# Performance work log

Measured on AMD Instinct MI355X. Metric: run time of the kernel, lower is better.

The kernel has to match this reference:

```python
import jax, jax.numpy as jnp
import numpy as np
from jax import lax

B, T, D, H = 128, 1024, 512, 512

def setup_inputs() -> dict:
    key = jax.random.key(0)
    k1, k2, k3 = jax.random.split(key, 3)
    sx = 1.0 / np.sqrt(D)
    sh = 1.0 / np.sqrt(H)
    return {
        "x": jax.random.normal(k1, (B, T, D), dtype=jnp.float32),
        "Wx": jax.random.normal(k2, (D, 4 * H), dtype=jnp.float32) * sx,
        "Wh": jax.random.normal(k3, (H, 4 * H), dtype=jnp.float32) * sh,
        "b": jnp.zeros((4 * H,), dtype=jnp.float32),
    }

def reference(x, Wx, Wh, b):
    # x: (B, T, D). Standard LSTM recurrence over time via lax.scan.
    batch = x.shape[0]
    hid = Wh.shape[0]
    h0 = jnp.zeros((batch, hid), dtype=x.dtype)
    c0 = jnp.zeros((batch, hid), dtype=x.dtype)
    # Precompute input projections for all timesteps (one big GEMM).
    xg = jnp.einsum('btd,dg->btg', x, Wx) + b  # (B, T, 4H)
    xg_t = jnp.transpose(xg, (1, 0, 2))        # (T, B, 4H)

    def step(carry, xg_step):
        h, c = carry
        gates = xg_step + h @ Wh               # (B, 4H)
        i, f, g, o = jnp.split(gates, 4, axis=-1)
        i = jax.nn.sigmoid(i)
        f = jax.nn.sigmoid(f)
        g = jnp.tanh(g)
        o = jax.nn.sigmoid(o)
        c_new = f * c + i * g
        h_new = o * jnp.tanh(c_new)
        return (h_new, c_new), h_new

    (final_h, final_c), _ = lax.scan(step, (h0, c0), xg_t)
    # return_sequences=False -> final hidden state
    return final_h
```

## Files before the change

### kernel.cpp

```cpp
#include <hip/hip_runtime.h>


typedef _Float16 f16;
typedef _Float16 f16x2 __attribute__((ext_vector_type(2)));
typedef _Float16 f16x8 __attribute__((ext_vector_type(8)));
typedef float f32x4 __attribute__((ext_vector_type(4)));
typedef unsigned u32x4 __attribute__((ext_vector_type(4)));

#define MFMA16(a, b, c) __builtin_amdgcn_mfma_f32_16x16x32_f16(a, b, c, 0, 0, 0)

__device__ __forceinline__ float sigf(float x) { return 1.0f / (1.0f + __expf(-x)); }
__device__ __forceinline__ float tanh_fast(float x) { return 1.0f - 2.0f / (__expf(2.0f * x) + 1.0f); }

#define OFF_WXT   0ull
#define OFF_WHT   2097152ull
#define OFF_HBUF  4194304ull
#define OFF_CST   4718592ull
#define OFF_XG    5242880ull

__global__ __launch_bounds__(256) void prep_kernel(
    const float* __restrict__ Wx, const float* __restrict__ Wh,
    f16* __restrict__ wxT, f16* __restrict__ whT,
    f16* __restrict__ hbuf, float* __restrict__ cst)
{
    unsigned i = blockIdx.x * 256u + threadIdx.x;
    if (i < 1048576u) {
        unsigned g = i >> 9, d = i & 511u;
        wxT[i] = (f16)Wx[d * 2048u + g];
        whT[i] = (f16)Wh[d * 2048u + g];
    }
    if (i < 131072u)
        ((unsigned*)hbuf)[i] = (i < 32768u) ? 0u : 0xFFFFFFFFu;
    if (i < 65536u) cst[i] = 0.0f;
}

__global__ __launch_bounds__(256) void gemm_xg(
    const float* __restrict__ x, const f16* __restrict__ wxT,
    const float* __restrict__ bias, f16* __restrict__ xg,
    int t0, int tcLog)
{
    __shared__ f16 smem[16384];
    f16* As = smem;
    f16* Bs = smem + 4096;

    const int tid = threadIdx.x;
    const int lane = tid & 63, wid = tid >> 6;
    const int wm = wid >> 1, wn = wid & 1;
    const int lr = lane & 15, lh = lane >> 4;
    const int n0 = blockIdx.x * 128;
    const long m0 = (long)blockIdx.y * 128;

    const int srow = tid >> 1;
    const int sc0_ = (tid & 1) * 2;
    const int swz = (srow >> 1) & 3;

    const long mg = m0 + srow;
    const long bb = mg >> tcLog;
    const long tl = mg & ((1L << tcLog) - 1);
    const float* xrow = x + ((bb * 1024 + t0 + tl) * 512 + sc0_ * 8);
    const f16* brow = wxT + ((long)(n0 + srow) * 512 + sc0_ * 8);

    f32x4 acc[4][4] = {};

    for (int k0 = 0; k0 < 512; k0 += 32) {
        __syncthreads();
        float4 a0 = *(const float4*)(xrow + k0);
        float4 a1 = *(const float4*)(xrow + k0 + 4);
        float4 a2 = *(const float4*)(xrow + k0 + 8);
        float4 a3 = *(const float4*)(xrow + k0 + 12);
        f16x8 ha, hb;
        ha[0] = (f16)a0.x; ha[1] = (f16)a0.y; ha[2] = (f16)a0.z; ha[3] = (f16)a0.w;
        ha[4] = (f16)a1.x; ha[5] = (f16)a1.y; ha[6] = (f16)a1.z; ha[7] = (f16)a1.w;
        hb[0] = (f16)a2.x; hb[1] = (f16)a2.y; hb[2] = (f16)a2.z; hb[3] = (f16)a2.w;
        hb[4] = (f16)a3.x; hb[5] = (f16)a3.y; hb[6] = (f16)a3.z; hb[7] = (f16)a3.w;
        *(f16x8*)(As + srow * 32 + ((sc0_    ) ^ swz) * 8) = ha;
        *(f16x8*)(As + srow * 32 + ((sc0_ + 1) ^ swz) * 8) = hb;
        f16x8 b0 = *(const f16x8*)(brow + k0);
        f16x8 b1 = *(const f16x8*)(brow + k0 + 8);
        *(f16x8*)(Bs + srow * 32 + ((sc0_    ) ^ swz) * 8) = b0;
        *(f16x8*)(Bs + srow * 32 + ((sc0_ + 1) ^ swz) * 8) = b1;
        __syncthreads();

        f16x8 af[4], bf[4];
        #pragma unroll
        for (int fm = 0; fm < 4; fm++) {
            int r = wm * 64 + fm * 16 + lr;
            af[fm] = *(const f16x8*)(As + r * 32 + (lh ^ ((r >> 1) & 3)) * 8);
        }
        #pragma unroll
        for (int fn = 0; fn < 4; fn++) {
            int r = wn * 64 + fn * 16 + lr;
            bf[fn] = *(const f16x8*)(Bs + r * 32 + (lh ^ ((r >> 1) & 3)) * 8);
        }
        #pragma unroll
        for (int fm = 0; fm < 4; fm++)
            #pragma unroll
            for (int fn = 0; fn < 4; fn++)
                acc[fm][fn] = MFMA16(af[fm], bf[fn], acc[fm][fn]);
    }

    __syncthreads();
    f16* Os = smem;
    #pragma unroll
    for (int fn = 0; fn < 4; fn++) {
        float bv = bias[n0 + wn * 64 + fn * 16 + lr];
        #pragma unroll
        for (int fm = 0; fm < 4; fm++) {
            #pragma unroll
            for (int r = 0; r < 4; r++) {
                int row = wm * 64 + fm * 16 + lh * 4 + r;
                int col = wn * 64 + fn * 16 + lr;
                Os[row * 128 + col] = (f16)(acc[fm][fn][r] + bv);
            }
        }
    }
    __syncthreads();
    const int orow = tid >> 1;
    const int ocol = (tid & 1) * 64;
    f16* dst = xg + (m0 + orow) * 2048 + n0 + ocol;
    const f16* srcp = Os + orow * 128 + ocol;
    #pragma unroll
    for (int j = 0; j < 8; j++)
        *(uint4*)(dst + j * 8) = *(const uint4*)(srcp + j * 8);
}

__global__ __launch_bounds__(256, 1) void lstm_rec(
    const f16* __restrict__ whT, const f16* __restrict__ xg,
    f16* __restrict__ hbuf, float* __restrict__ cst,
    float* __restrict__ out, int t0, int tcLog)
{
    __shared__ unsigned short hA[16 * 520];
    __shared__ float gl[2048];
    const int tid = threadIdx.x;
    const int lane = tid & 63, w = tid >> 6;
    const int lr = lane & 15, lh = lane >> 4;
    const int g = blockIdx.x & 7, s = blockIdx.x >> 3;
    const int Tc = 1 << tcLog;

    f16x8 breg[2][16];
    #pragma unroll
    for (int fn = 0; fn < 2; fn++) {
        const f16* wp = whT + (long)(w * 512 + s * 32 + fn * 16 + lr) * 512 + lh * 8;
        #pragma unroll
        for (int ks = 0; ks < 16; ks++)
            breg[fn][ks] = *(const f16x8*)(wp + ks * 32);
    }

    const int pb = tid >> 4;
    const int pu = (tid & 15) * 2;
    const int bg = g * 16 + pb;
    const int hcol = s * 32 + pu;
    float2 cc = *(const float2*)(cst + bg * 512 + hcol);

    const int r_ = lane >> 2, cq_ = lane & 3;
    const long goff = (long)(g * 16 + r_) * 512 + w * 128 + cq_ * 8;

    const f16* xbase = xg + ((long)(bg << tcLog)) * 2048 + hcol;
    f16x2 xv0 = *(const f16x2*)(xbase);
    f16x2 xv1 = *(const f16x2*)(xbase + 512);
    f16x2 xv2 = *(const f16x2*)(xbase + 1024);
    f16x2 xv3 = *(const f16x2*)(xbase + 1536);

    for (int t = 0; t < Tc; t++) {
        const int tt = t0 + t;

        const f16* gq = hbuf + (tt & 3) * 65536 + goff;
        f16x8 q0, q1, q2, q3;
        int guard = 0;
        for (;;) {
            asm volatile("global_load_dwordx4 %0, %1, off sc0 sc1" : "=v"(q0) : "v"(gq) : "memory");
            asm volatile("global_load_dwordx4 %0, %1, off sc0 sc1" : "=v"(q1) : "v"(gq + 32) : "memory");
            asm volatile("global_load_dwordx4 %0, %1, off sc0 sc1" : "=v"(q2) : "v"(gq + 64) : "memory");
            asm volatile("global_load_dwordx4 %0, %1, off sc0 sc1" : "=v"(q3) : "v"(gq + 96) : "memory");
            asm volatile("s_waitcnt vmcnt(0)" ::: "memory");
            __builtin_amdgcn_sched_barrier(0);
            unsigned mx = 0u;
            {
                u32x4 u = __builtin_bit_cast(u32x4, q0);
                asm("v_pk_max_u16 %0, %0, %1" : "+v"(mx) : "v"(u.x));
                asm("v_pk_max_u16 %0, %0, %1" : "+v"(mx) : "v"(u.y));
                asm("v_pk_max_u16 %0, %0, %1" : "+v"(mx) : "v"(u.z));
                asm("v_pk_max_u16 %0, %0, %1" : "+v"(mx) : "v"(u.w));
            }
            {
                u32x4 u = __builtin_bit_cast(u32x4, q1);
                asm("v_pk_max_u16 %0, %0, %1" : "+v"(mx) : "v"(u.x));
                asm("v_pk_max_u16 %0, %0, %1" : "+v"(mx) : "v"(u.y));
                asm("v_pk_max_u16 %0, %0, %1" : "+v"(mx) : "v"(u.z));
                asm("v_pk_max_u16 %0, %0, %1" : "+v"(mx) : "v"(u.w));
            }
            {
                u32x4 u = __builtin_bit_cast(u32x4, q2);
                asm("v_pk_max_u16 %0, %0, %1" : "+v"(mx) : "v"(u.x));
                asm("v_pk_max_u16 %0, %0, %1" : "+v"(mx) : "v"(u.y));
                asm("v_pk_max_u16 %0, %0, %1" : "+v"(mx) : "v"(u.z));
                asm("v_pk_max_u16 %0, %0, %1" : "+v"(mx) : "v"(u.w));
            }
            {
                u32x4 u = __builtin_bit_cast(u32x4, q3);
                asm("v_pk_max_u16 %0, %0, %1" : "+v"(mx) : "v"(u.x));
                asm("v_pk_max_u16 %0, %0, %1" : "+v"(mx) : "v"(u.y));
                asm("v_pk_max_u16 %0, %0, %1" : "+v"(mx) : "v"(u.z));
                asm("v_pk_max_u16 %0, %0, %1" : "+v"(mx) : "v"(u.w));
            }
            int ok = ((mx & 0xFFFFu) != 0xFFFFu) && ((mx >> 16) != 0xFFFFu);
            if (__all(ok) || ++guard > 5000) break;
        }

        {
            unsigned short* dst = hA + r_ * 520 + w * 128 + cq_ * 8;
            *(f16x8*)(dst     ) = q0;
            *(f16x8*)(dst + 32) = q1;
            *(f16x8*)(dst + 64) = q2;
            *(f16x8*)(dst + 96) = q3;
        }
        __syncthreads();

        {
            f16* pz = hbuf + ((tt + 2) & 3) * 65536 + bg * 512 + hcol;
            unsigned cany = 0xFFFFFFFFu;
            asm volatile("global_store_dword %0, %1, off sc0 sc1"
                         :: "v"(pz), "v"(cany) : "memory");
        }

        f32x4 acc0 = {0.f, 0.f, 0.f, 0.f}, acc1 = {0.f, 0.f, 0.f, 0.f};
        #pragma unroll
        for (int ks = 0; ks < 16; ks++) {
            f16x8 a = *(const f16x8*)(hA + lr * 520 + lh * 8 + ks * 32);
            acc0 = MFMA16(a, breg[0][ks], acc0);
            acc1 = MFMA16(a, breg[1][ks], acc1);
        }
        #pragma unroll
        for (int r = 0; r < 4; r++) {
            gl[w * 512 + (lh * 4 + r) * 32 + lr] = acc0[r];
            gl[w * 512 + (lh * 4 + r) * 32 + 16 + lr] = acc1[r];
        }
        __syncthreads();

        float2 gi = *(const float2*)(gl + 0 * 512 + pb * 32 + pu);
        float2 gf = *(const float2*)(gl + 1 * 512 + pb * 32 + pu);
        float2 gg = *(const float2*)(gl + 2 * 512 + pb * 32 + pu);
        float2 go = *(const float2*)(gl + 3 * 512 + pb * 32 + pu);
        float i0 = sigf(gi.x + (float)xv0[0]);
        float i1 = sigf(gi.y + (float)xv0[1]);
        float f0 = sigf(gf.x + (float)xv1[0]);
        float f1 = sigf(gf.y + (float)xv1[1]);
        float g0 = tanh_fast(gg.x + (float)xv2[0]);
        float g1 = tanh_fast(gg.y + (float)xv2[1]);
        float o0 = sigf(go.x + (float)xv3[0]);
        float o1 = sigf(go.y + (float)xv3[1]);
        cc.x = f0 * cc.x + i0 * g0;
        cc.y = f1 * cc.y + i1 * g1;
        float h0 = o0 * tanh_fast(cc.x);
        float h1 = o1 * tanh_fast(cc.y);

        asm volatile("s_waitcnt vmcnt(0)" ::: "memory");
        {
            f16* hd = hbuf + ((tt + 1) & 3) * 65536 + bg * 512 + hcol;
            union { f16x2 h; unsigned u; } cv;
            cv.h[0] = (f16)h0; cv.h[1] = (f16)h1;
            asm volatile("global_store_dword %0, %1, off sc0 sc1"
                         :: "v"(hd), "v"(cv.u) : "memory");
        }
        if (tt == 1023) *(float2*)(out + bg * 512 + hcol) = make_float2(h0, h1);

        if (t + 1 < Tc) {
            const f16* xr = xbase + (long)(t + 1) * 2048;
            xv0 = *(const f16x2*)(xr);
            xv1 = *(const f16x2*)(xr + 512);
            xv2 = *(const f16x2*)(xr + 1024);
            xv3 = *(const f16x2*)(xr + 1536);
        }
    }
    *(float2*)(cst + bg * 512 + hcol) = cc;
}

extern "C" void kernel_launch(void* const* d_in, const int* in_sizes, int n_in,
                              void* d_out, int out_size, void* d_ws, size_t ws_size,
                              hipStream_t stream)
{
    const float* x    = (const float*)d_in[0];
    const float* Wx   = (const float*)d_in[1];
    const float* Wh   = (const float*)d_in[2];
    const float* bias = (const float*)d_in[3];
    float* out = (float*)d_out;
    char* ws = (char*)d_ws;

    f16*      wxT   = (f16*)(ws + OFF_WXT);
    f16*      whT   = (f16*)(ws + OFF_WHT);
    f16*      hbuf  = (f16*)(ws + OFF_HBUF);
    float*    cst   = (float*)(ws + OFF_CST);
    f16*      xgb   = (f16*)(ws + OFF_XG);

    int tcLog = 10;
    while (tcLog > 0 && OFF_XG + (524288ull << tcLog) > ws_size) tcLog--;
    const int nch = 1024 >> tcLog;

    prep_kernel<<<4096, 256, 0, stream>>>(Wx, Wh, wxT, whT, hbuf, cst);

    for (int c = 0; c < nch; c++) {
        int t0 = c << tcLog;
        dim3 gA(16, 1u << tcLog);
        gemm_xg<<<gA, 256, 0, stream>>>(x, wxT, bias, xgb, t0, tcLog);

        const f16* whT_a = whT; const f16* xg_a = xgb; f16* hbuf_a = hbuf;
        float* cst_a = cst; float* out_a = out;
        int t0_a = t0, tcl_a = tcLog;
        void* args[7] = { &whT_a, &xg_a, &hbuf_a, &cst_a, &out_a, &t0_a, &tcl_a };
        if (hipLaunchCooperativeKernel((const void*)lstm_rec, dim3(128), dim3(256),
                                       args, 0, stream) != hipSuccess) {
            lstm_rec<<<dim3(128), dim3(256), 0, stream>>>(whT, xgb, hbuf, cst, out, t0, tcLog);
        }
    }
}
```

Measured before the change: 3.424 ms.

## Deepen h ring buffer to 8 slots, drop store fence, pad gate LDS

Grows the global hidden-state ring buffer from 4 to 8 slots and invalidates the slot three steps ahead instead of two. This lets the s_waitcnt vmcnt(0) before the h store be removed, since the sentinel write and the data write can no longer race on the same slot. It also pads the gate scratch in LDS to a stride of 33 to avoid bank conflicts, at the cost of splitting each float2 read into scalar reads. The memory layout offsets move to make room for the larger buffer.

```diff
diff --git a/kernel.cpp b/kernel.cpp
--- a/kernel.cpp
+++ b/kernel.cpp
@@ -15,8 +15,8 @@
 #define OFF_WXT   0ull
 #define OFF_WHT   2097152ull
 #define OFF_HBUF  4194304ull
-#define OFF_CST   4718592ull
-#define OFF_XG    5242880ull
+#define OFF_CST   5242880ull
+#define OFF_XG    5505024ull
 
 __global__ __launch_bounds__(256) void prep_kernel(
     const float* __restrict__ Wx, const float* __restrict__ Wh,
@@ -29,7 +29,7 @@
         wxT[i] = (f16)Wx[d * 2048u + g];
         whT[i] = (f16)Wh[d * 2048u + g];
     }
-    if (i < 131072u)
+    if (i < 262144u)
         ((unsigned*)hbuf)[i] = (i < 32768u) ? 0u : 0xFFFFFFFFu;
     if (i < 65536u) cst[i] = 0.0f;
 }
@@ -124,13 +124,20 @@
         *(uint4*)(dst + j * 8) = *(const uint4*)(srcp + j * 8);
 }
 
+#define VALIDATE16(mx, q)                                            \
+    {  u32x4 u = __builtin_bit_cast(u32x4, q);                       \
+       asm("v_pk_max_u16 %0, %0, %1" : "+v"(mx) : "v"(u.x));         \
+       asm("v_pk_max_u16 %0, %0, %1" : "+v"(mx) : "v"(u.y));         \
+       asm("v_pk_max_u16 %0, %0, %1" : "+v"(mx) : "v"(u.z));         \
+       asm("v_pk_max_u16 %0, %0, %1" : "+v"(mx) : "v"(u.w));  }
+
 __global__ __launch_bounds__(256, 1) void lstm_rec(
     const f16* __restrict__ whT, const f16* __restrict__ xg,
     f16* __restrict__ hbuf, float* __restrict__ cst,
     float* __restrict__ out, int t0, int tcLog)
 {
     __shared__ unsigned short hA[16 * 520];
-    __shared__ float gl[2048];
+    __shared__ float gl[4 * 528];
     const int tid = threadIdx.x;
     const int lane = tid & 63, w = tid >> 6;
     const int lr = lane & 15, lh = lane >> 4;
@@ -164,7 +171,7 @@
     for (int t = 0; t < Tc; t++) {
         const int tt = t0 + t;
 
-        const f16* gq = hbuf + (tt & 3) * 65536 + goff;
+        const f16* gq = hbuf + (tt & 7) * 65536 + goff;
         f16x8 q0, q1, q2, q3;
         int guard = 0;
         for (;;) {
@@ -175,34 +182,7 @@
             asm volatile("s_waitcnt vmcnt(0)" ::: "memory");
             __builtin_amdgcn_sched_barrier(0);
             unsigned mx = 0u;
-            {
-                u32x4 u = __builtin_bit_cast(u32x4, q0);
-                asm("v_pk_max_u16 %0, %0, %1" : "+v"(mx) : "v"(u.x));
-                asm("v_pk_max_u16 %0, %0, %1" : "+v"(mx) : "v"(u.y));
-                asm("v_pk_max_u16 %0, %0, %1" : "+v"(mx) : "v"(u.z));
-                asm("v_pk_max_u16 %0, %0, %1" : "+v"(mx) : "v"(u.w));
-            }
-            {
-                u32x4 u = __builtin_bit_cast(u32x4, q1);
-                asm("v_pk_max_u16 %0, %0, %1" : "+v"(mx) : "v"(u.x));
-                asm("v_pk_max_u16 %0, %0, %1" : "+v"(mx) : "v"(u.y));
-                asm("v_pk_max_u16 %0, %0, %1" : "+v"(mx) : "v"(u.z));
-                asm("v_pk_max_u16 %0, %0, %1" : "+v"(mx) : "v"(u.w));
-            }
-            {
-                u32x4 u = __builtin_bit_cast(u32x4, q2);
-                asm("v_pk_max_u16 %0, %0, %1" : "+v"(mx) : "v"(u.x));
-                asm("v_pk_max_u16 %0, %0, %1" : "+v"(mx) : "v"(u.y));
-                asm("v_pk_max_u16 %0, %0, %1" : "+v"(mx) : "v"(u.z));
-                asm("v_pk_max_u16 %0, %0, %1" : "+v"(mx) : "v"(u.w));
-            }
-            {
-                u32x4 u = __builtin_bit_cast(u32x4, q3);
-                asm("v_pk_max_u16 %0, %0, %1" : "+v"(mx) : "v"(u.x));
-                asm("v_pk_max_u16 %0, %0, %1" : "+v"(mx) : "v"(u.y));
-                asm("v_pk_max_u16 %0, %0, %1" : "+v"(mx) : "v"(u.z));
-                asm("v_pk_max_u16 %0, %0, %1" : "+v"(mx) : "v"(u.w));
-            }
+            VALIDATE16(mx, q0) VALIDATE16(mx, q1) VALIDATE16(mx, q2) VALIDATE16(mx, q3)
             int ok = ((mx & 0xFFFFu) != 0xFFFFu) && ((mx >> 16) != 0xFFFFu);
             if (__all(ok) || ++guard > 5000) break;
         }
@@ -217,7 +197,7 @@
         __syncthreads();
 
         {
-            f16* pz = hbuf + ((tt + 2) & 3) * 65536 + bg * 512 + hcol;
+            f16* pz = hbuf + ((tt + 3) & 7) * 65536 + bg * 512 + hcol;
             unsigned cany = 0xFFFFFFFFu;
             asm volatile("global_store_dword %0, %1, off sc0 sc1"
                          :: "v"(pz), "v"(cany) : "memory");
@@ -232,31 +212,30 @@
         }
         #pragma unroll
         for (int r = 0; r < 4; r++) {
-            gl[w * 512 + (lh * 4 + r) * 32 + lr] = acc0[r];
-            gl[w * 512 + (lh * 4 + r) * 32 + 16 + lr] = acc1[r];
-        }
-        __syncthreads();
-
-        float2 gi = *(const float2*)(gl + 0 * 512 + pb * 32 + pu);
-        float2 gf = *(const float2*)(gl + 1 * 512 + pb * 32 + pu);
-        float2 gg = *(const float2*)(gl + 2 * 512 + pb * 32 + pu);
-        float2 go = *(const float2*)(gl + 3 * 512 + pb * 32 + pu);
-        float i0 = sigf(gi.x + (float)xv0[0]);
-        float i1 = sigf(gi.y + (float)xv0[1]);
-        float f0 = sigf(gf.x + (float)xv1[0]);
-        float f1 = sigf(gf.y + (float)xv1[1]);
-        float g0 = tanh_fast(gg.x + (float)xv2[0]);
-        float g1 = tanh_fast(gg.y + (float)xv2[1]);
-        float o0 = sigf(go.x + (float)xv3[0]);
-        float o1 = sigf(go.y + (float)xv3[1]);
+            gl[w * 528 + (lh * 4 + r) * 33 + lr] = acc0[r];
+            gl[w * 528 + (lh * 4 + r) * 33 + 16 + lr] = acc1[r];
+        }
+        __syncthreads();
+
+        float gi0 = gl[0 * 528 + pb * 33 + pu], gi1 = gl[0 * 528 + pb * 33 + pu + 1];
+        float gf0 = gl[1 * 528 + pb * 33 + pu], gf1 = gl[1 * 528 + pb * 33 + pu + 1];
+        float gg0 = gl[2 * 528 + pb * 33 + pu], gg1 = gl[2 * 528 + pb * 33 + pu + 1];
+        float go0 = gl[3 * 528 + pb * 33 + pu], go1 = gl[3 * 528 + pb * 33 + pu + 1];
+        float i0 = sigf(gi0 + (float)xv0[0]);
+        float i1 = sigf(gi1 + (float)xv0[1]);
+        float f0 = sigf(gf0 + (float)xv1[0]);
+        float f1 = sigf(gf1 + (float)xv1[1]);
+        float g0 = tanh_fast(gg0 + (float)xv2[0]);
+        float g1 = tanh_fast(gg1 + (float)xv2[1]);
+        float o0 = sigf(go0 + (float)xv3[0]);
+        float o1 = sigf(go1 + (float)xv3[1]);
         cc.x = f0 * cc.x + i0 * g0;
         cc.y = f1 * cc.y + i1 * g1;
         float h0 = o0 * tanh_fast(cc.x);
         float h1 = o1 * tanh_fast(cc.y);
 
-        asm volatile("s_waitcnt vmcnt(0)" ::: "memory");
         {
-            f16* hd = hbuf + ((tt + 1) & 3) * 65536 + bg * 512 + hcol;
+            f16* hd = hbuf + ((tt + 1) & 7) * 65536 + bg * 512 + hcol;
             union { f16x2 h; unsigned u; } cv;
             cv.h[0] = (f16)h0; cv.h[1] = (f16)h1;
             asm volatile("global_store_dword %0, %1, off sc0 sc1"
```

Result: no change. 3.437 ms (+0.4%).
